# Kernel tuning notes

Hardware: AMD Instinct MI355X
Metric: run time of the kernel (lower is better)

## Reference

```python
import jax, jax.numpy as jnp
import numpy as np

N, E, IN_DIM, OUT_DIM, NNZ = 4096, 2048, 256, 256, 65536
ALPHA = 0.2          # LeakyReLU negative slope
NEG_GAT = -9e15      # masked_fill value for GAT adjacency mask
NEG_ATT = -1e9       # masked_fill value inside ScaledDotProductAttention_hyper


def setup_inputs() -> dict:
    key = jax.random.key(0)
    ks = jax.random.split(key, 10)
    stdv = 1.0 / np.sqrt(OUT_DIM)
    u = lambda k, shape: jax.random.uniform(k, shape, jnp.float32, -stdv, stdv)
    x = jax.random.normal(ks[0], (N, IN_DIM), jnp.float32)
    node_idx = jax.random.randint(ks[1], (NNZ,), 0, N, jnp.int32)
    edge_idx = jax.random.randint(ks[2], (NNZ,), 0, E, jnp.int32)
    hyperedge_index = jnp.stack([node_idx, edge_idx])  # [2, NNZ]
    return {
        "x": x,
        "weight": u(ks[3], (IN_DIM, OUT_DIM)),
        "weight2": u(ks[4], (IN_DIM, OUT_DIM)),
        "weight3": u(ks[5], (OUT_DIM, OUT_DIM)),
        "weight_g": u(ks[6], (IN_DIM, OUT_DIM)),
        "a_g": u(ks[7], (2 * OUT_DIM, 1)),
        "word_context": u(ks[8], (1, OUT_DIM)),
        "bias": u(ks[9], (OUT_DIM,)),
        "hyperedge_index": hyperedge_index,
        "num_edges": E,
    }


def reference(x, weight, weight2, weight3, weight_g, a_g, word_context, bias,
              hyperedge_index, num_edges):
    n = x.shape[0]
    d = weight_g.shape[1]
    temp = d ** 0.5  # temperature = out_features ** 0.5

    # --- hypergraph preprocessing: dense incidence H [N, E] and node adjacency A [N, N]
    H = jnp.zeros((n, num_edges), x.dtype).at[hyperedge_index[0], hyperedge_index[1]].set(1.0)
    A = (H @ H.T > 0).astype(x.dtype)
    A = A.at[jnp.arange(n), jnp.arange(n)].set(1.0)  # fill_diagonal_(1)

    # --- dense GAT-style attention over the clique-expanded graph
    Wh_g = x @ weight_g                               # [N, D]
    Wh1 = Wh_g @ a_g[:d]                              # [N, 1]
    Wh2 = Wh_g @ a_g[d:]                              # [N, 1]
    e_g = jax.nn.leaky_relu(Wh1 + Wh2.T, ALPHA)       # [N, N]
    attention_g = jax.nn.softmax(jnp.where(A > 0, e_g, NEG_GAT), axis=1)

    # --- project node-node attention onto hyperedges: [N, E]
    graph2hyper = attention_g @ H

    # --- dual hypergraph cross-attention (eval mode: dropout is identity)
    x_4att = x @ weight2                              # [N, D]
    xw = x @ weight + bias                            # [N, D] (transfer=True)

    # attention1: hyperedge queries attend over nodes, mask = H.T [E, N]
    q1 = jnp.broadcast_to(word_context[0], (num_edges, d))
    attn1 = (q1 / temp) @ x_4att.T                    # [E, N]
    attn1 = jnp.where(H.T == 0, NEG_ATT, attn1)
    att1 = jax.nn.softmax(graph2hyper.T, axis=-1) + jax.nn.softmax(attn1, axis=-1)
    edge = att1 @ xw                                  # [E, D]
    att2he = att1.T                                   # [N, E]

    # attention2: node queries attend over hyperedges, mask = H [N, E]
    edge_4att = edge @ weight3                        # [E, D]
    attn2 = (x_4att / temp) @ edge_4att.T             # [N, E]
    attn2 = jnp.where(H == 0, NEG_ATT, attn2)
    att2hn = jax.nn.softmax(graph2hyper, axis=-1) + jax.nn.softmax(attn2, axis=-1)
    node = att2hn @ edge                              # [N, D]

    # --- combine attentions and aggregate
    att2_he_out = att2he @ att2he.T                   # [N, N]
    att2_hn_out = att2hn @ att2hn.T                   # [N, N]
    attention_out = attention_g + att2_he_out + att2_hn_out
    h_prime_g = jax.nn.elu(attention_out @ Wh_g)      # concat=True -> ELU

    node = jax.nn.relu(node)                          # concat=True -> ReLU, then squeeze
    return node, h_prime_g
```

## Files before the change

### kernel.cpp

```cpp
#include <hip/hip_runtime.h>
#include <cstdint>
#include <cstddef>


#define DI __device__ __forceinline__
typedef unsigned short u16;
typedef unsigned int   u32;
typedef __bf16 bf16x8 __attribute__((ext_vector_type(8)));
typedef float  f32x4  __attribute__((ext_vector_type(4)));
typedef u32    u32x4  __attribute__((ext_vector_type(4)));

constexpr int NN  = 4096;
constexpr int EE  = 2048;
constexpr int NNZb = 65536;

constexpr size_t MB = (size_t)1 << 20;
constexpr size_t OFF_HBITS   = 0;
constexpr size_t OFF_HBITST  = 1*MB;
constexpr size_t OFF_ABITS   = 2*MB;
constexpr size_t OFF_EDGE    = 2*MB;
constexpr size_t OFF_WH1     = 4*MB;
constexpr size_t OFF_WH2     = 4*MB + 16384;
constexpr size_t OFF_V       = 4*MB + 32768;
constexpr size_t OFF_RSINV   = 4*MB + 49152;
constexpr size_t OFF_WCAT    = 5*MB;
constexpr size_t OFF_XB      = 6*MB;
constexpr size_t OFF_EDGET   = 6*MB;
constexpr size_t OFF_HN2T    = 7*MB;
constexpr size_t OFF_WHG     = 8*MB;
constexpr size_t OFF_X4ATT   = 10*MB;
constexpr size_t OFF_YB      = 12*MB;
constexpr size_t OFF_XWT     = 14*MB;
constexpr size_t OFF_WHGTA   = 16*MB;
constexpr size_t OFF_HBT     = 18*MB;
constexpr size_t OFF_EDGE2T  = 18*MB;
constexpr size_t OFF_WHGTB   = 34*MB;
constexpr size_t OFF_EXPA    = 36*MB;
constexpr size_t OFF_ATT1    = 36*MB;
constexpr size_t OFF_ATT2HN  = 36*MB;
constexpr size_t OFF_ATT1T   = 52*MB;
constexpr size_t OFF_G2H     = 68*MB;
constexpr size_t OFF_G2HT    = 84*MB;
constexpr size_t OFF_ATT2HNT = 84*MB;
constexpr size_t OFF_ATTN2   = 100*MB;
constexpr size_t OFF_G1      = 116*MB;
constexpr size_t OFF_C2      = 120*MB;

DI u16 to_bf(float f) {
  union { float f; u32 u; } x; x.f = f;
  u32 r = x.u + 0x7fffu + ((x.u >> 16) & 1u);
  return (u16)(r >> 16);
}
DI float from_bf(u16 h) { union { u32 u; float f; } x; x.u = (u32)h << 16; return x.f; }
DI void store_bf4(u16* p, float a, float b, float c, float d) {
  u32 lo = (u32)to_bf(a) | ((u32)to_bf(b) << 16);
  u32 hi = (u32)to_bf(c) | ((u32)to_bf(d) << 16);
  *(u32*)p = lo; *((u32*)p + 1) = hi;
}

DI float wredf(float v) {
  #pragma unroll
  for (int o = 32; o; o >>= 1) v += __shfl_down(v, o);
  return v;
}
DI int wredi(int v) {
  #pragma unroll
  for (int o = 32; o; o >>= 1) v += __shfl_down(v, o);
  return v;
}

typedef __attribute__((address_space(3))) void lds_void;
typedef __attribute__((address_space(1))) void glb_void;
DI void async_load16(const void* g, void* l) {
  __builtin_amdgcn_global_load_lds((glb_void*)(uintptr_t)g,
                                   (lds_void*)(u32)(uintptr_t)l, 16, 0, 0);
}

template <int BM, int BN, class Epi>
DI void gemm_body(const u16* __restrict__ A, const u16* __restrict__ B,
                  int nb, int K, Epi epi, int tile, u16* As, u16* Bs)
{
  constexpr int BK = 64;
  constexpr int WM = BM / 2, WN = BN / 2;
  constexpr int FM = WM / 16, FN = WN / 16;
  constexpr int AI = (BM * 8) / 256, BI = (BN * 8) / 256;

  const int tid = threadIdx.x;
  const int w = tid >> 6, l = tid & 63;
  const int bi = tile / nb, bj = tile - bi * nb;
  const int i0 = bi * BM, j0 = bj * BN;
  const int wm = (w & 1) * WM, wn = (w >> 1) * WN;
  const int quad = l >> 4, m16 = l & 15;

  f32x4 acc[FM][FN] = {};

  for (int kb = 0; kb < K; kb += BK) {
    __syncthreads();
    #pragma unroll
    for (int i = 0; i < AI; ++i) {
      const int ci = (i * 4 + w) * 64 + l;
      const int r = ci >> 3;
      const int lc = (ci & 7) ^ (r & 7);
      async_load16(A + (size_t)(i0 + r) * K + kb + lc * 8, &As[(i * 4 + w) * 512]);
    }
    #pragma unroll
    for (int i = 0; i < BI; ++i) {
      const int ci = (i * 4 + w) * 64 + l;
      const int r = ci >> 3;
      const int lc = (ci & 7) ^ (r & 7);
      async_load16(B + (size_t)(j0 + r) * K + kb + lc * 8, &Bs[(i * 4 + w) * 512]);
    }
    __syncthreads();
    #pragma unroll
    for (int ks = 0; ks < 2; ++ks) {
      bf16x8 af[FM], bfv[FN];
      #pragma unroll
      for (int mi = 0; mi < FM; ++mi) {
        const int row = wm + mi * 16 + m16;
        af[mi] = *(const bf16x8*)&As[row * BK + (((ks * 4 + quad) ^ (row & 7)) * 8)];
      }
      #pragma unroll
      for (int ni = 0; ni < FN; ++ni) {
        const int row = wn + ni * 16 + m16;
        bfv[ni] = *(const bf16x8*)&Bs[row * BK + (((ks * 4 + quad) ^ (row & 7)) * 8)];
      }
      #pragma unroll
      for (int mi = 0; mi < FM; ++mi)
        #pragma unroll
        for (int ni = 0; ni < FN; ++ni)
          acc[mi][ni] = __builtin_amdgcn_mfma_f32_16x16x32_bf16(
              af[mi], bfv[ni], acc[mi][ni], 0, 0, 0);
    }
  }
  #pragma unroll
  for (int mi = 0; mi < FM; ++mi)
    #pragma unroll
    for (int ni = 0; ni < FN; ++ni) {
      const int rb = i0 + wm + mi * 16 + quad * 4;
      const int c  = j0 + wn + ni * 16 + m16;
      epi(rb, c, acc[mi][ni]);
    }
}

DI void t32_tile(const u16* __restrict__ in, u16* __restrict__ out,
                 int R, int C, int bx, int by, u16* t) {
  int tx = threadIdx.x & 31, ty = threadIdx.x >> 5;
  int x0 = bx * 32, y0 = by * 32;
  #pragma unroll
  for (int k = 0; k < 32; k += 8)
    t[(ty + k) * 33 + tx] = in[(size_t)(y0 + ty + k) * C + x0 + tx];
  __syncthreads();
  #pragma unroll
  for (int k = 0; k < 32; k += 8)
    out[(size_t)(x0 + ty + k) * R + y0 + tx] = t[tx * 33 + ty + k];
}

struct EpiG0 {
  u16 *whg, *whgTa, *whgTb, *x4, *xwT; const float* bias;
  DI void operator()(int r, int c, f32x4 v) const {
    if (c < 256) {
      #pragma unroll
      for (int i = 0; i < 4; ++i) whg[(r + i) * 256 + c] = to_bf(v[i]);
      store_bf4(&whgTa[(size_t)c * NN + r], v[0], v[1], v[2], v[3]);
      store_bf4(&whgTb[(size_t)c * NN + r], v[0], v[1], v[2], v[3]);
    } else if (c < 512) {
      #pragma unroll
      for (int i = 0; i < 4; ++i) x4[(r + i) * 256 + (c - 256)] = to_bf(v[i]);
    } else {
      float b = bias[c - 512];
      store_bf4(&xwT[(size_t)(c - 512) * NN + r], v[0]+b, v[1]+b, v[2]+b, v[3]+b);
    }
  }
};
struct EpiBig {
  const float* rsInv; u16* g2h; u16* g2hT; float* g1;
  DI void operator()(int r, int c, f32x4 v) const {
    float w0 = v[0]*rsInv[r], w1 = v[1]*rsInv[r+1], w2 = v[2]*rsInv[r+2], w3 = v[3]*rsInv[r+3];
    if (c < 2048) {
      g2h[(size_t)r * EE + c] = to_bf(w0);
      g2h[(size_t)(r+1) * EE + c] = to_bf(w1);
      g2h[(size_t)(r+2) * EE + c] = to_bf(w2);
      g2h[(size_t)(r+3) * EE + c] = to_bf(w3);
      store_bf4(&g2hT[(size_t)c * NN + r], w0, w1, w2, w3);
    } else {
      g1[(r) * 256 + (c - 2048)] = w0;
      g1[(r+1) * 256 + (c - 2048)] = w1;
      g1[(r+2) * 256 + (c - 2048)] = w2;
      g1[(r+3) * 256 + (c - 2048)] = w3;
    }
  }
};
struct EpiEdgeT {
  u16 *edgeT, *edge2T, *edge;
  DI void operator()(int r, int c, f32x4 v) const {
    if (r < 256) {
      #pragma unroll
      for (int i = 0; i < 4; ++i) edgeT[(size_t)(r + i) * EE + c] = to_bf(v[i]);
      store_bf4(&edge[(size_t)c * 256 + r], v[0], v[1], v[2], v[3]);
    } else {
      #pragma unroll
      for (int i = 0; i < 4; ++i) edge2T[(size_t)(r - 256 + i) * EE + c] = to_bf(v[i]);
    }
  }
};
struct EpiCombine {
  const float* g1; const float* c2; float* out;
  DI void operator()(int r, int c, f32x4 v) const {
    if (c < 256) {
      #pragma unroll
      for (int i = 0; i < 4; ++i) out[(r + i) * 256 + c] = fmaxf(v[i], 0.f);
    } else {
      int d = c - 256;
      #pragma unroll
      for (int i = 0; i < 4; ++i) {
        float s = g1[(r + i) * 256 + d] + c2[(r + i) * 256 + d] + v[i];
        out[1048576 + (r + i) * 256 + d] = s > 0.f ? s : expm1f(s);
      }
    }
  }
};
struct EpiBf16 { u16* out; int ldn;
  DI void operator()(int r, int c, f32x4 v) const {
    #pragma unroll
    for (int i = 0; i < 4; ++i) out[(size_t)(r + i) * ldn + c] = to_bf(v[i]);
  } };
struct EpiBf16Scale { u16* out; int ldn; float s;
  DI void operator()(int r, int c, f32x4 v) const {
    #pragma unroll
    for (int i = 0; i < 4; ++i) out[(size_t)(r + i) * ldn + c] = to_bf(v[i] * s);
  } };
struct EpiF32 { float* out; int ldn;
  DI void operator()(int r, int c, f32x4 v) const {
    #pragma unroll
    for (int i = 0; i < 4; ++i) out[(size_t)(r + i) * ldn + c] = v[i];
  } };

template <int BM, int BN, int LB, class Epi>
__global__ __launch_bounds__(256, LB)
void gemm_k(const u16* __restrict__ A, const u16* __restrict__ B,
            int nb, int K, Epi epi) {
  __shared__ __align__(16) u16 smem[(BM + BN) * 64];
  gemm_body<BM, BN>(A, B, nb, K, epi, blockIdx.x, smem, smem + BM * 64);
}

__global__ __launch_bounds__(256, 2)
void k_tri_edge(const u16* __restrict__ Fcat, const u16* __restrict__ Att1,
                EpiEdgeT e0,
                const u16* __restrict__ X4att, const u16* __restrict__ W3b,
                EpiBf16 e1,
                const u16* __restrict__ tin, u16* __restrict__ tout) {
  __shared__ __align__(16) u16 smem[192 * 64];
  int b = blockIdx.x;
  if (b < 256)      gemm_body<64, 64>(Fcat, Att1, 32, 4096, e0, b, smem, smem + 64 * 64);
  else if (b < 384) gemm_body<128, 64>(X4att, W3b, 4, 256, e1, b - 256, smem, smem + 128 * 64);
  else { int t = b - 384; t32_tile(tin, tout, EE, NN, t & 127, t >> 7, smem); }
}

__global__ __launch_bounds__(256, 2)
void k_dual_attn2(const u16* __restrict__ Att1T, const u16* __restrict__ Edge2T,
                  EpiF32 e0,
                  const u16* __restrict__ Yb, const u16* __restrict__ Edge,
                  EpiBf16Scale e1) {
  __shared__ __align__(16) u16 smem[256 * 64];
  int b = blockIdx.x;
  if (b < 128) gemm_body<128, 64>(Att1T, Edge2T, 4, 2048, e0, b, smem, smem + 128 * 64);
  else         gemm_body<128, 128>(Yb, Edge, 16, 256, e1, b - 128, smem, smem + 128 * 64);
}

__global__ void k_prep(const float* wg, const float* w2, const float* w1,
                       const float* w3, const float* x, u16* wcat, u16* xb,
                       char* zbits, char* zhbt) {
  int idx = blockIdx.x * 256 + threadIdx.x;
  if (blockIdx.x < 5120) {
    if (idx < 196608) {
      int blk = idx >> 16, r = idx & 65535;
      int d = r >> 8, kk = r & 255;
      const float* src = blk == 0 ? wg : blk == 1 ? w2 : w1;
      wcat[idx] = to_bf(src[kk * 256 + d]);
    } else if (idx < 262144) {
      int r = idx - 196608;
      wcat[196608 + r] = to_bf(w3[r]);
    } else {
      int r = idx - 262144;
      xb[r] = to_bf(x[r]);
    }
  } else {
    int z = idx - 5120 * 256;
    u32x4 zero = {0, 0, 0, 0};
    if (z < 262144) ((u32x4*)zbits)[z] = zero;
    else            ((u32x4*)zhbt)[z - 262144] = zero;
  }
}

__global__ void k_scatter_diag(const int* __restrict__ hidx, u32* hbits, u32* hbitsT,
                               u16* hbT, u32* abits) {
  int k = blockIdx.x * 256 + threadIdx.x;
  if (k < NNZb) {
    int n = hidx[k], e = hidx[NNZb + k];
    atomicOr(&hbits[n * 64 + (e >> 5)], 1u << (e & 31));
    atomicOr(&hbitsT[e * 128 + (n >> 5)], 1u << (n & 31));
    hbT[(size_t)e * NN + n] = 0x3F80;
  } else {
    int i = k - NNZb;
    if (i < NN) atomicOr(&abits[i * 128 + (i >> 5)], 1u << (i & 31));
  }
}

__global__ void k_rowclique(const u16* __restrict__ whg, const u16* __restrict__ x4,
                            const float* __restrict__ ag, const float* __restrict__ wc,
                            float* wh1, float* wh2, float* v,
                            const u32* __restrict__ hbitsT, u32* abits) {
  __shared__ int list[512];
  __shared__ int cnt;
  int tid = threadIdx.x;
  if (blockIdx.x < 1024) {
    int wv = tid >> 6, l = tid & 63;
    int row = blockIdx.x * 4 + wv;
    float s1 = 0, s2 = 0, s3 = 0;
    #pragma unroll
    for (int dd = 0; dd < 4; ++dd) {
      int d = l * 4 + dd;
      float a = from_bf(whg[row * 256 + d]);
      s1 += a * ag[d]; s2 += a * ag[256 + d];
      s3 += from_bf(x4[row * 256 + d]) * wc[d];
    }
    s1 = wredf(s1); s2 = wredf(s2); s3 = wredf(s3);
    if (l == 0) { wh1[row] = s1; wh2[row] = s2; v[row] = s3 * (1.0f / 16.0f); }
  } else {
    int e = blockIdx.x - 1024;
    if (tid == 0) cnt = 0;
    __syncthreads();
    if (tid < 128) {
      u32 w = hbitsT[e * 128 + tid];
      while (w) {
        int b = __ffs(w) - 1;
        int p = atomicAdd(&cnt, 1);
        if (p < 512) list[p] = tid * 32 + b;
        w &= w - 1;
      }
    }
    __syncthreads();
    int c = cnt < 512 ? cnt : 512;
    for (int p = tid; p < c * c; p += 256) {
      int i = list[p / c], j = list[p % c];
      atomicOr(&abits[i * 128 + (j >> 5)], 1u << (j & 31));
    }
  }
}

__global__ void k_exprows(const u32* __restrict__ abits, const float* __restrict__ wh1,
                          const float* __restrict__ wh2, u16* __restrict__ expA,
                          float* rsInv) {
  int i = blockIdx.x, tid = threadIdx.x;
  __shared__ float w2s[NN];
  __shared__ float ssum;
  for (int j = tid; j < NN; j += 256) w2s[j] = wh2[j];
  if (tid == 0) ssum = 0.f;
  __syncthreads();
  float a = wh1[i], lsum = 0.f;
  for (int j = tid; j < NN; j += 256) {
    u32 w = abits[i * 128 + (j >> 5)];
    u16 h = 0;
    if ((w >> (j & 31)) & 1) {
      float z = a + w2s[j];
      float eg = z > 0.f ? z : 0.2f * z;
      h = to_bf(__expf(eg));
      lsum += from_bf(h);
    }
    expA[(size_t)i * NN + j] = h;
  }
  lsum = wredf(lsum);
  if ((tid & 63) == 0) atomicAdd(&ssum, lsum);
  __syncthreads();
  if (tid == 0) rsInv[i] = 1.0f / ssum;
}

__global__ void k_edge_softmax(const u16* __restrict__ g2hT, const u32* __restrict__ hbitsT,
                               const float* __restrict__ v, u16* __restrict__ att1) {
  int e = blockIdx.x, tid = threadIdx.x;
  __shared__ float evals[NN];
  __shared__ u32 hw[128];
  __shared__ float s1s, s2s; __shared__ int cs;
  if (tid == 0) { s1s = 0.f; s2s = 0.f; cs = 0; }
  if (tid < 128) hw[tid] = hbitsT[e * 128 + tid];
  __syncthreads();
  float sum1 = 0.f;
  for (int j = tid; j < NN; j += 256) {
    float ev = __expf(from_bf(g2hT[(size_t)e * NN + j]));
    evals[j] = ev; sum1 += ev;
  }
  float sum2 = 0.f; int cnt = 0;
  if (tid < 128) {
    u32 w = hw[tid]; cnt = __popc(w);
    while (w) { int b = __ffs(w) - 1; sum2 += __expf(v[tid * 32 + b]); w &= w - 1; }
  }
  sum1 = wredf(sum1); sum2 = wredf(sum2); cnt = wredi(cnt);
  if ((tid & 63) == 0) { atomicAdd(&s1s, sum1); atomicAdd(&s2s, sum2); atomicAdd(&cs, cnt); }
  __syncthreads();
  float inv1 = 1.0f / s1s;
  int c = cs;
  float inv2 = c > 0 ? 1.0f / s2s : 0.0f;
  float unif = c > 0 ? 0.0f : (1.0f / (float)NN);
  for (int j = tid; j < NN; j += 256) {
    float t = evals[j] * inv1 + unif;
    if ((hw[j >> 5] >> (j & 31)) & 1) t += __expf(v[j]) * inv2;
    att1[(size_t)e * NN + j] = to_bf(t);
  }
}

__global__ void k_node_softmax(const u16* __restrict__ g2h, const u16* __restrict__ attn2,
                               const u32* __restrict__ hbits, u16* __restrict__ att2hn) {
  int n = blockIdx.x, tid = threadIdx.x;
  __shared__ float ev3[EE], ev4[EE];
  __shared__ u32 hw[64];
  __shared__ float s3s, s4s; __shared__ int cs;
  if (tid == 0) { s3s = 0.f; s4s = 0.f; cs = 0; }
  if (tid < 64) hw[tid] = hbits[n * 64 + tid];
  __syncthreads();
  float s3 = 0.f, s4 = 0.f; int cl = 0;
  for (int e = tid; e < EE; e += 256) {
    float x3 = __expf(from_bf(g2h[(size_t)n * EE + e]));
    ev3[e] = x3; s3 += x3;
    bool m = (hw[e >> 5] >> (e & 31)) & 1;
    float x4 = m ? __expf(from_bf(attn2[(size_t)n * EE + e])) : 0.f;
    ev4[e] = x4; s4 += x4; cl += m;
  }
  s3 = wredf(s3); s4 = wredf(s4); cl = wredi(cl);
  if ((tid & 63) == 0) { atomicAdd(&s3s, s3); atomicAdd(&s4s, s4); atomicAdd(&cs, cl); }
  __syncthreads();
  float inv3 = 1.0f / s3s;
  int c = cs;
  float inv4 = c > 0 ? 1.0f / s4s : 0.0f;
  float unif = c > 0 ? 0.0f : (1.0f / (float)EE);
  for (int e = tid; e < EE; e += 256)
    att2hn[(size_t)n * EE + e] = to_bf(ev3[e] * inv3 + ev4[e] * inv4 + unif);
}

__global__ void k_transpose(const u16* __restrict__ in, u16* __restrict__ out,
                            int R, int C) {
  __shared__ u16 t[32 * 33];
  t32_tile(in, out, R, C, blockIdx.x, blockIdx.y, t);
}

extern "C" void kernel_launch(void* const* d_in, const int* in_sizes, int n_in,
                              void* d_out, int out_size, void* d_ws, size_t ws_size,
                              hipStream_t stream) {
  (void)in_sizes; (void)n_in; (void)out_size; (void)ws_size;
  const float* x    = (const float*)d_in[0];
  const float* w1   = (const float*)d_in[1];
  const float* w2   = (const float*)d_in[2];
  const float* w3   = (const float*)d_in[3];
  const float* wg   = (const float*)d_in[4];
  const float* ag   = (const float*)d_in[5];
  const float* wc   = (const float*)d_in[6];
  const float* bias = (const float*)d_in[7];
  const int*   hidx = (const int*)d_in[8];
  float* out = (float*)d_out;
  char* ws = (char*)d_ws;

  u32* Hbits   = (u32*)(ws + OFF_HBITS);
  u32* HbitsT  = (u32*)(ws + OFF_HBITST);
  u32* Abits   = (u32*)(ws + OFF_ABITS);
  float* Wh1   = (float*)(ws + OFF_WH1);
  float* Wh2   = (float*)(ws + OFF_WH2);
  float* V     = (float*)(ws + OFF_V);
  float* RsInv = (float*)(ws + OFF_RSINV);
  u16* Wcat    = (u16*)(ws + OFF_WCAT);
  u16* W3b     = Wcat + 196608;
  u16* Xb      = (u16*)(ws + OFF_XB);
  u16* Whg     = (u16*)(ws + OFF_WHG);
  u16* X4att   = (u16*)(ws + OFF_X4ATT);
  u16* Yb      = (u16*)(ws + OFF_YB);
  u16* XwT     = (u16*)(ws + OFF_XWT);
  u16* WhgTa   = (u16*)(ws + OFF_WHGTA);
  u16* HbT     = (u16*)(ws + OFF_HBT);
  u16* WhgTb   = (u16*)(ws + OFF_WHGTB);
  u16* ExpA    = (u16*)(ws + OFF_EXPA);
  u16* Att1    = (u16*)(ws + OFF_ATT1);
  u16* Att1T   = (u16*)(ws + OFF_ATT1T);
  u16* Att2hn  = (u16*)(ws + OFF_ATT2HN);
  u16* G2h     = (u16*)(ws + OFF_G2H);
  u16* G2hT    = (u16*)(ws + OFF_G2HT);
  u16* Att2hnT = (u16*)(ws + OFF_ATT2HNT);
  u16* Attn2   = (u16*)(ws + OFF_ATTN2);
  float* G1    = (float*)(ws + OFF_G1);
  float* C2    = (float*)(ws + OFF_C2);
  u16* Edge    = (u16*)(ws + OFF_EDGE);
  u16* EdgeT   = (u16*)(ws + OFF_EDGET);
  u16* Hn2T    = (u16*)(ws + OFF_HN2T);
  u16* Edge2T  = (u16*)(ws + OFF_EDGE2T);

  k_prep<<<10240, 256, 0, stream>>>(wg, w2, w1, w3, x, Wcat, Xb,
                                    ws + OFF_HBITS, ws + OFF_HBT);
  k_scatter_diag<<<272, 256, 0, stream>>>(hidx, Hbits, HbitsT, HbT, Abits);
  gemm_k<128, 64, 3><<<384, 256, 0, stream>>>(
      Xb, Wcat, 12, 256, EpiG0{Whg, WhgTa, WhgTb, X4att, XwT, bias});
  k_rowclique<<<3072, 256, 0, stream>>>(Whg, X4att, ag, wc, Wh1, Wh2, V,
                                        HbitsT, Abits);
  k_exprows<<<NN, 256, 0, stream>>>(Abits, Wh1, Wh2, ExpA, RsInv);
  gemm_k<128, 96, 3><<<768, 256, 0, stream>>>(
      ExpA, HbT, 24, NN, EpiBig{RsInv, G2h, G2hT, G1});
  k_edge_softmax<<<EE, 256, 0, stream>>>(G2hT, HbitsT, V, Att1);
  k_tri_edge<<<8576, 256, 0, stream>>>(
      XwT, Att1, EpiEdgeT{EdgeT, Edge2T, Edge},
      X4att, W3b, EpiBf16{Yb, 256},
      Att1, Att1T);
  k_dual_attn2<<<640, 256, 0, stream>>>(
      Att1T, Edge2T, EpiF32{C2, 256},
      Yb, Edge, EpiBf16Scale{Attn2, EE, 1.0f / 16.0f});
  k_node_softmax<<<NN, 256, 0, stream>>>(G2h, Attn2, Hbits, Att2hn);
  k_transpose<<<dim3(64, 128), 256, 0, stream>>>(Att2hn, Att2hnT, NN, EE);
  gemm_k<64, 32, 2><<<256, 256, 0, stream>>>(
      WhgTa, Att2hnT, 64, NN, EpiBf16{Hn2T, EE});
  gemm_k<64, 64, 2><<<512, 256, 0, stream>>>(
      Att2hn, EdgeT, 8, EE, EpiCombine{G1, C2, out});
}
```

Before: 395.0 us.

## Replace dense ExpA×H GEMM with sparse per-edge gather and split-K Hn2 GEMM

Drops the dense bf16 incidence matrix HbT and the large ExpA@[H|WhgT] GEMM. A new k_sparse kernel builds exp-rows for 8 nodes per block in LDS and gathers graph2hyper through per-edge member lists produced in k_rowclique. G1 moves to a separate unnormalised GEMM whose row scaling happens in the combine epilogue, and that GEMM is fused with the edge softmax in one launch. The WhgT·Att2hnT GEMM becomes split-K with float atomics plus a cast kernel. Member lists are capped at 64 per half-edge, which could truncate in unusual inputs, and the atomics add nondeterminism.

Result: slower. 403.5 us (+2.2%).

```diff
diff --git a/kernel.cpp b/kernel.cpp
--- a/kernel.cpp
+++ b/kernel.cpp
@@ -32,16 +32,17 @@
 constexpr size_t OFF_YB      = 12*MB;
 constexpr size_t OFF_XWT     = 14*MB;
 constexpr size_t OFF_WHGTA   = 16*MB;
-constexpr size_t OFF_HBT     = 18*MB;
 constexpr size_t OFF_EDGE2T  = 18*MB;
-constexpr size_t OFF_WHGTB   = 34*MB;
+constexpr size_t OFF_GLISTS  = 19*MB;
+constexpr size_t OFF_CNT2    = 19*MB + 524288;
+constexpr size_t OFF_HN2ACC  = 34*MB;
 constexpr size_t OFF_EXPA    = 36*MB;
-constexpr size_t OFF_ATT1    = 36*MB;
 constexpr size_t OFF_ATT2HN  = 36*MB;
 constexpr size_t OFF_ATT1T   = 52*MB;
 constexpr size_t OFF_G2H     = 68*MB;
 constexpr size_t OFF_G2HT    = 84*MB;
 constexpr size_t OFF_ATT2HNT = 84*MB;
+constexpr size_t OFF_ATT1    = 100*MB;
 constexpr size_t OFF_ATTN2   = 100*MB;
 constexpr size_t OFF_G1      = 116*MB;
 constexpr size_t OFF_C2      = 120*MB;
@@ -52,6 +53,8 @@
   return (u16)(r >> 16);
 }
 DI float from_bf(u16 h) { union { u32 u; float f; } x; x.u = (u32)h << 16; return x.f; }
+DI float bflo(u32 u) { union { u32 u; float f; } x; x.u = u << 16; return x.f; }
+DI float bfhi(u32 u) { union { u32 u; float f; } x; x.u = u & 0xffff0000u; return x.f; }
 DI void store_bf4(u16* p, float a, float b, float c, float d) {
   u32 lo = (u32)to_bf(a) | ((u32)to_bf(b) << 16);
   u32 hi = (u32)to_bf(c) | ((u32)to_bf(d) << 16);
@@ -78,7 +81,8 @@
 
 template <int BM, int BN, class Epi>
 DI void gemm_body(const u16* __restrict__ A, const u16* __restrict__ B,
-                  int nb, int K, Epi epi, int tile, u16* As, u16* Bs)
+                  int nb, int K, int k0, int kLen, Epi epi, int tile,
+                  u16* As, u16* Bs)
 {
   constexpr int BK = 64;
   constexpr int WM = BM / 2, WN = BN / 2;
@@ -94,7 +98,7 @@
 
   f32x4 acc[FM][FN] = {};
 
-  for (int kb = 0; kb < K; kb += BK) {
+  for (int kb = k0; kb < k0 + kLen; kb += BK) {
     __syncthreads();
     #pragma unroll
     for (int i = 0; i < AI; ++i) {
@@ -156,13 +160,12 @@
 }
 
 struct EpiG0 {
-  u16 *whg, *whgTa, *whgTb, *x4, *xwT; const float* bias;
+  u16 *whg, *whgTa, *x4, *xwT; const float* bias;
   DI void operator()(int r, int c, f32x4 v) const {
     if (c < 256) {
       #pragma unroll
       for (int i = 0; i < 4; ++i) whg[(r + i) * 256 + c] = to_bf(v[i]);
       store_bf4(&whgTa[(size_t)c * NN + r], v[0], v[1], v[2], v[3]);
-      store_bf4(&whgTb[(size_t)c * NN + r], v[0], v[1], v[2], v[3]);
     } else if (c < 512) {
       #pragma unroll
       for (int i = 0; i < 4; ++i) x4[(r + i) * 256 + (c - 256)] = to_bf(v[i]);
@@ -172,24 +175,6 @@
     }
   }
 };
-struct EpiBig {
-  const float* rsInv; u16* g2h; u16* g2hT; float* g1;
-  DI void operator()(int r, int c, f32x4 v) const {
-    float w0 = v[0]*rsInv[r], w1 = v[1]*rsInv[r+1], w2 = v[2]*rsInv[r+2], w3 = v[3]*rsInv[r+3];
-    if (c < 2048) {
-      g2h[(size_t)r * EE + c] = to_bf(w0);
-      g2h[(size_t)(r+1) * EE + c] = to_bf(w1);
-      g2h[(size_t)(r+2) * EE + c] = to_bf(w2);
-      g2h[(size_t)(r+3) * EE + c] = to_bf(w3);
-      store_bf4(&g2hT[(size_t)c * NN + r], w0, w1, w2, w3);
-    } else {
-      g1[(r) * 256 + (c - 2048)] = w0;
-      g1[(r+1) * 256 + (c - 2048)] = w1;
-      g1[(r+2) * 256 + (c - 2048)] = w2;
-      g1[(r+3) * 256 + (c - 2048)] = w3;
-    }
-  }
-};
 struct EpiEdgeT {
   u16 *edgeT, *edge2T, *edge;
   DI void operator()(int r, int c, f32x4 v) const {
@@ -204,7 +189,7 @@
   }
 };
 struct EpiCombine {
-  const float* g1; const float* c2; float* out;
+  const float* g1; const float* c2; const float* rsInv; float* out;
   DI void operator()(int r, int c, f32x4 v) const {
     if (c < 256) {
       #pragma unroll
@@ -213,7 +198,7 @@
       int d = c - 256;
       #pragma unroll
       for (int i = 0; i < 4; ++i) {
-        float s = g1[(r + i) * 256 + d] + c2[(r + i) * 256 + d] + v[i];
+        float s = g1[(r + i) * 256 + d] * rsInv[r + i] + c2[(r + i) * 256 + d] + v[i];
         out[1048576 + (r + i) * 256 + d] = s > 0.f ? s : expm1f(s);
       }
     }
@@ -234,42 +219,27 @@
     #pragma unroll
     for (int i = 0; i < 4; ++i) out[(size_t)(r + i) * ldn + c] = v[i];
   } };
-
-template <int BM, int BN, int LB, class Epi>
+struct EpiAtomF32 { float* out; int ldn;
+  DI void operator()(int r, int c, f32x4 v) const {
+    #pragma unroll
+    for (int i = 0; i < 4; ++i) atomicAdd(&out[(size_t)(r + i) * ldn + c], v[i]);
+  } };
+
+template <int BM, int BN, int S, int LB, class Epi>
 __global__ __launch_bounds__(256, LB)
 void gemm_k(const u16* __restrict__ A, const u16* __restrict__ B,
             int nb, int K, Epi epi) {
   __shared__ __align__(16) u16 smem[(BM + BN) * 64];
-  gemm_body<BM, BN>(A, B, nb, K, epi, blockIdx.x, smem, smem + BM * 64);
-}
-
-__global__ __launch_bounds__(256, 2)
-void k_tri_edge(const u16* __restrict__ Fcat, const u16* __restrict__ Att1,
-                EpiEdgeT e0,
-                const u16* __restrict__ X4att, const u16* __restrict__ W3b,
-                EpiBf16 e1,
-                const u16* __restrict__ tin, u16* __restrict__ tout) {
-  __shared__ __align__(16) u16 smem[192 * 64];
-  int b = blockIdx.x;
-  if (b < 256)      gemm_body<64, 64>(Fcat, Att1, 32, 4096, e0, b, smem, smem + 64 * 64);
-  else if (b < 384) gemm_body<128, 64>(X4att, W3b, 4, 256, e1, b - 256, smem, smem + 128 * 64);
-  else { int t = b - 384; t32_tile(tin, tout, EE, NN, t & 127, t >> 7, smem); }
-}
-
-__global__ __launch_bounds__(256, 2)
-void k_dual_attn2(const u16* __restrict__ Att1T, const u16* __restrict__ Edge2T,
-                  EpiF32 e0,
-                  const u16* __restrict__ Yb, const u16* __restrict__ Edge,
-                  EpiBf16Scale e1) {
-  __shared__ __align__(16) u16 smem[256 * 64];
-  int b = blockIdx.x;
-  if (b < 128) gemm_body<128, 64>(Att1T, Edge2T, 4, 2048, e0, b, smem, smem + 128 * 64);
-  else         gemm_body<128, 128>(Yb, Edge, 16, 256, e1, b - 128, smem, smem + 128 * 64);
+  const int tilesPer = gridDim.x / S;
+  int t = blockIdx.x;
+  const int s = t / tilesPer; t -= s * tilesPer;
+  const int kLen = K / S;
+  gemm_body<BM, BN>(A, B, nb, K, s * kLen, kLen, epi, t, smem, smem + BM * 64);
 }
 
 __global__ void k_prep(const float* wg, const float* w2, const float* w1,
                        const float* w3, const float* x, u16* wcat, u16* xb,
-                       char* zbits, char* zhbt) {
+                       char* zbits, char* zhn2) {
   int idx = blockIdx.x * 256 + threadIdx.x;
   if (blockIdx.x < 5120) {
     if (idx < 196608) {
@@ -288,18 +258,17 @@
     int z = idx - 5120 * 256;
     u32x4 zero = {0, 0, 0, 0};
     if (z < 262144) ((u32x4*)zbits)[z] = zero;
-    else            ((u32x4*)zhbt)[z - 262144] = zero;
+    else            ((u32x4*)zhn2)[z - 262144] = zero;
   }
 }
 
 __global__ void k_scatter_diag(const int* __restrict__ hidx, u32* hbits, u32* hbitsT,
-                               u16* hbT, u32* abits) {
+                               u32* abits) {
   int k = blockIdx.x * 256 + threadIdx.x;
   if (k < NNZb) {
     int n = hidx[k], e = hidx[NNZb + k];
     atomicOr(&hbits[n * 64 + (e >> 5)], 1u << (e & 31));
     atomicOr(&hbitsT[e * 128 + (n >> 5)], 1u << (n & 31));
-    hbT[(size_t)e * NN + n] = 0x3F80;
   } else {
     int i = k - NNZb;
     if (i < NN) atomicOr(&abits[i * 128 + (i >> 5)], 1u << (i & 31));
@@ -309,9 +278,11 @@
 __global__ void k_rowclique(const u16* __restrict__ whg, const u16* __restrict__ x4,
                             const float* __restrict__ ag, const float* __restrict__ wc,
                             float* wh1, float* wh2, float* v,
-                            const u32* __restrict__ hbitsT, u32* abits) {
+                            const u32* __restrict__ hbitsT, u32* abits,
+                            u16* glists, u32* cnt2) {
   __shared__ int list[512];
   __shared__ int cnt;
+  __shared__ u32 c2[2];
   int tid = threadIdx.x;
   if (blockIdx.x < 1024) {
     int wv = tid >> 6, l = tid & 63;
@@ -329,17 +300,23 @@
   } else {
     int e = blockIdx.x - 1024;
     if (tid == 0) cnt = 0;
+    if (tid < 2) c2[tid] = 0;
     __syncthreads();
     if (tid < 128) {
       u32 w = hbitsT[e * 128 + tid];
+      int p = tid >> 6;
       while (w) {
         int b = __ffs(w) - 1;
-        int p = atomicAdd(&cnt, 1);
-        if (p < 512) list[p] = tid * 32 + b;
+        int n = tid * 32 + b;
+        int q = atomicAdd(&cnt, 1);
+        if (q < 512) list[q] = n;
+        u32 s = atomicAdd(&c2[p], 1u);
+        if (s < 64) glists[(e * 2 + p) * 64 + s] = (u16)n;
         w &= w - 1;
       }
     }
     __syncthreads();
+    if (tid < 2) cnt2[e * 2 + tid] = c2[tid] < 64u ? c2[tid] : 64u;
     int c = cnt < 512 ? cnt : 512;
     for (int p = tid; p < c * c; p += 256) {
       int i = list[p / c], j = list[p % c];
@@ -348,40 +325,95 @@
   }
 }
 
-__global__ void k_exprows(const u32* __restrict__ abits, const float* __restrict__ wh1,
-                          const float* __restrict__ wh2, u16* __restrict__ expA,
-                          float* rsInv) {
-  int i = blockIdx.x, tid = threadIdx.x;
-  __shared__ float w2s[NN];
-  __shared__ float ssum;
-  for (int j = tid; j < NN; j += 256) w2s[j] = wh2[j];
-  if (tid == 0) ssum = 0.f;
-  __syncthreads();
-  float a = wh1[i], lsum = 0.f;
-  for (int j = tid; j < NN; j += 256) {
-    u32 w = abits[i * 128 + (j >> 5)];
-    u16 h = 0;
-    if ((w >> (j & 31)) & 1) {
-      float z = a + w2s[j];
-      float eg = z > 0.f ? z : 0.2f * z;
-      h = to_bf(__expf(eg));
-      lsum += from_bf(h);
-    }
-    expA[(size_t)i * NN + j] = h;
-  }
-  lsum = wredf(lsum);
-  if ((tid & 63) == 0) atomicAdd(&ssum, lsum);
-  __syncthreads();
-  if (tid == 0) rsInv[i] = 1.0f / ssum;
-}
-
-__global__ void k_edge_softmax(const u16* __restrict__ g2hT, const u32* __restrict__ hbitsT,
-                               const float* __restrict__ v, u16* __restrict__ att1) {
-  int e = blockIdx.x, tid = threadIdx.x;
-  __shared__ float evals[NN];
-  __shared__ u32 hw[128];
-  __shared__ float s1s, s2s; __shared__ int cs;
-  if (tid == 0) { s1s = 0.f; s2s = 0.f; cs = 0; }
+__global__ __launch_bounds__(256, 2)
+void k_sparse(const u32* __restrict__ abits, const float* __restrict__ wh1,
+              const float* __restrict__ wh2, const u16* __restrict__ glists,
+              const u32* __restrict__ cnt2, u16* __restrict__ expA,
+              float* __restrict__ rsInv, u16* __restrict__ g2h,
+              u16* __restrict__ g2hT)
+{
+  __shared__ u16 lds[2048 * 12];
+  __shared__ float sums8[8], rsi[8];
+  const int tid = threadIdx.x;
+  const int i0 = blockIdx.x * 8;
+  const int r = tid & 7, ng = tid >> 3;
+  if (tid < 8) sums8[tid] = 0.f;
+  float acc[8][8] = {};
+  const float wh1r = wh1[i0 + r];
+  for (int p = 0; p < 2; ++p) {
+    __syncthreads();
+    float partial = 0.f;
+    for (int it = 0; it < 8; ++it) {
+      const int g = ng + 32 * it;
+      const int n0 = p * 2048 + g * 8;
+      const u32 m8 = (abits[(size_t)(i0 + r) * 128 + (n0 >> 5)] >> (n0 & 31)) & 0xffu;
+      u32 pk[4];
+      #pragma unroll
+      for (int q = 0; q < 4; ++q) {
+        u32 wrd = 0;
+        #pragma unroll
+        for (int h = 0; h < 2; ++h) {
+          const int j = q * 2 + h;
+          u16 hb = 0;
+          if ((m8 >> j) & 1u) {
+            float z = wh1r + wh2[n0 + j];
+            float eg = z > 0.f ? z : 0.2f * z;
+            hb = to_bf(__expf(eg));
+            partial += from_bf(hb);
+          }
+          lds[(g * 8 + j) * 12 + r] = hb;
+          wrd |= (u32)hb << (16 * h);
+        }
+        pk[q] = wrd;
+      }
+      *(u32x4*)&expA[(size_t)(i0 + r) * 4096 + n0] = u32x4{pk[0], pk[1], pk[2], pk[3]};
+    }
+    atomicAdd(&sums8[r], partial);
+    __syncthreads();
+    #pragma unroll
+    for (int j = 0; j < 8; ++j) {
+      const int e = tid + 256 * j;
+      const int c = (int)cnt2[e * 2 + p];
+      const u16* lst = &glists[(e * 2 + p) * 64];
+      for (int k = 0; k < c; ++k) {
+        const int ln = (int)lst[k] - p * 2048;
+        const u32* lp = (const u32*)&lds[ln * 12];
+        u32 a0 = lp[0], a1 = lp[1], a2 = lp[2], a3 = lp[3];
+        acc[j][0] += bflo(a0); acc[j][1] += bfhi(a0);
+        acc[j][2] += bflo(a1); acc[j][3] += bfhi(a1);
+        acc[j][4] += bflo(a2); acc[j][5] += bfhi(a2);
+        acc[j][6] += bflo(a3); acc[j][7] += bfhi(a3);
+      }
+    }
+  }
+  __syncthreads();
+  if (tid < 8) {
+    float s = 1.f / sums8[tid];
+    rsi[tid] = s; rsInv[i0 + tid] = s;
+  }
+  __syncthreads();
+  #pragma unroll
+  for (int j = 0; j < 8; ++j) {
+    const int e = tid + 256 * j;
+    u32 pk[4];
+    #pragma unroll
+    for (int q = 0; q < 4; ++q) {
+      u16 lo = to_bf(acc[j][2 * q] * rsi[2 * q]);
+      u16 hi = to_bf(acc[j][2 * q + 1] * rsi[2 * q + 1]);
+      pk[q] = (u32)lo | ((u32)hi << 16);
+      g2h[(size_t)(i0 + 2 * q) * EE + e] = lo;
+      g2h[(size_t)(i0 + 2 * q + 1) * EE + e] = hi;
+    }
+    *(u32x4*)&g2hT[(size_t)e * NN + i0] = u32x4{pk[0], pk[1], pk[2], pk[3]};
+  }
+}
+
+DI void edge_softmax_body(int e, const u16* __restrict__ g2hT,
+                          const u32* __restrict__ hbitsT,
+                          const float* __restrict__ v, u16* __restrict__ att1,
+                          float* evals, u32* hw, float* s1s, float* s2s, int* cs) {
+  int tid = threadIdx.x;
+  if (tid == 0) { *s1s = 0.f; *s2s = 0.f; *cs = 0; }
   if (tid < 128) hw[tid] = hbitsT[e * 128 + tid];
   __syncthreads();
   float sum1 = 0.f;
@@ -395,17 +427,58 @@
     while (w) { int b = __ffs(w) - 1; sum2 += __expf(v[tid * 32 + b]); w &= w - 1; }
   }
   sum1 = wredf(sum1); sum2 = wredf(sum2); cnt = wredi(cnt);
-  if ((tid & 63) == 0) { atomicAdd(&s1s, sum1); atomicAdd(&s2s, sum2); atomicAdd(&cs, cnt); }
-  __syncthreads();
-  float inv1 = 1.0f / s1s;
-  int c = cs;
-  float inv2 = c > 0 ? 1.0f / s2s : 0.0f;
+  if ((tid & 63) == 0) { atomicAdd(s1s, sum1); atomicAdd(s2s, sum2); atomicAdd(cs, cnt); }
+  __syncthreads();
+  float inv1 = 1.0f / *s1s;
+  int c = *cs;
+  float inv2 = c > 0 ? 1.0f / *s2s : 0.0f;
   float unif = c > 0 ? 0.0f : (1.0f / (float)NN);
   for (int j = tid; j < NN; j += 256) {
     float t = evals[j] * inv1 + unif;
     if ((hw[j >> 5] >> (j & 31)) & 1) t += __expf(v[j]) * inv2;
     att1[(size_t)e * NN + j] = to_bf(t);
   }
+}
+
+__global__ __launch_bounds__(256, 2)
+void k_dual_g1(const u16* __restrict__ ExpA, const u16* __restrict__ WhgTa,
+               EpiF32 eg,
+               const u16* __restrict__ g2hT, const u32* __restrict__ hbitsT,
+               const float* __restrict__ v, u16* __restrict__ att1) {
+  __shared__ __align__(16) char buf[24576];
+  __shared__ float s1s, s2s; __shared__ int cs;
+  int b = blockIdx.x;
+  if (b < 128) {
+    u16* As = (u16*)buf;
+    gemm_body<128, 64>(ExpA, WhgTa, 4, NN, 0, NN, eg, b, As, As + 128 * 64);
+  } else {
+    edge_softmax_body(b - 128, g2hT, hbitsT, v, att1,
+                      (float*)buf, (u32*)(buf + 16384), &s1s, &s2s, &cs);
+  }
+}
+
+__global__ __launch_bounds__(256, 2)
+void k_tri_edge(const u16* __restrict__ Fcat, const u16* __restrict__ Att1,
+                EpiEdgeT e0,
+                const u16* __restrict__ X4att, const u16* __restrict__ W3b,
+                EpiBf16 e1,
+                const u16* __restrict__ tin, u16* __restrict__ tout) {
+  __shared__ __align__(16) u16 smem[192 * 64];
+  int b = blockIdx.x;
+  if (b < 256)      gemm_body<64, 64>(Fcat, Att1, 32, NN, 0, NN, e0, b, smem, smem + 64 * 64);
+  else if (b < 384) gemm_body<128, 64>(X4att, W3b, 4, 256, 0, 256, e1, b - 256, smem, smem + 128 * 64);
+  else { int t = b - 384; t32_tile(tin, tout, EE, NN, t & 127, t >> 7, smem); }
+}
+
+__global__ __launch_bounds__(256, 2)
+void k_dual_attn2(const u16* __restrict__ Att1T, const u16* __restrict__ Edge2T,
+                  EpiF32 e0,
+                  const u16* __restrict__ Yb, const u16* __restrict__ Edge,
+                  EpiBf16Scale e1) {
+  __shared__ __align__(16) u16 smem[256 * 64];
+  int b = blockIdx.x;
+  if (b < 128) gemm_body<128, 64>(Att1T, Edge2T, 4, EE, 0, EE, e0, b, smem, smem + 128 * 64);
+  else         gemm_body<128, 128>(Yb, Edge, 16, 256, 0, 256, e1, b - 128, smem, smem + 128 * 64);
 }
 
 __global__ void k_node_softmax(const u16* __restrict__ g2h, const u16* __restrict__ attn2,
@@ -440,6 +513,11 @@
                             int R, int C) {
   __shared__ u16 t[32 * 33];
   t32_tile(in, out, R, C, blockIdx.x, blockIdx.y, t);
+}
+
+__global__ void k_cast_hn2(const float* __restrict__ acc, u16* __restrict__ hn2T) {
+  int idx = blockIdx.x * 256 + threadIdx.x;
+  hn2T[idx] = to_bf(acc[idx]);
 }
 
 extern "C" void kernel_launch(void* const* d_in, const int* in_sizes, int n_in,
@@ -473,34 +551,35 @@
   u16* Yb      = (u16*)(ws + OFF_YB);
   u16* XwT     = (u16*)(ws + OFF_XWT);
   u16* WhgTa   = (u16*)(ws + OFF_WHGTA);
-  u16* HbT     = (u16*)(ws + OFF_HBT);
-  u16* WhgTb   = (u16*)(ws + OFF_WHGTB);
+  u16* Edge2T  = (u16*)(ws + OFF_EDGE2T);
+  u16* Glists  = (u16*)(ws + OFF_GLISTS);
+  u32* Cnt2    = (u32*)(ws + OFF_CNT2);
+  float* Hn2Acc = (float*)(ws + OFF_HN2ACC);
   u16* ExpA    = (u16*)(ws + OFF_EXPA);
-  u16* Att1    = (u16*)(ws + OFF_ATT1);
+  u16* Att2hn  = (u16*)(ws + OFF_ATT2HN);
   u16* Att1T   = (u16*)(ws + OFF_ATT1T);
-  u16* Att2hn  = (u16*)(ws + OFF_ATT2HN);
   u16* G2h     = (u16*)(ws + OFF_G2H);
   u16* G2hT    = (u16*)(ws + OFF_G2HT);
   u16* Att2hnT = (u16*)(ws + OFF_ATT2HNT);
+  u16* Att1    = (u16*)(ws + OFF_ATT1);
   u16* Attn2   = (u16*)(ws + OFF_ATTN2);
   float* G1    = (float*)(ws + OFF_G1);
   float* C2    = (float*)(ws + OFF_C2);
   u16* Edge    = (u16*)(ws + OFF_EDGE);
   u16* EdgeT   = (u16*)(ws + OFF_EDGET);
   u16* Hn2T    = (u16*)(ws + OFF_HN2T);
-  u16* Edge2T  = (u16*)(ws + OFF_EDGE2T);
-
-  k_prep<<<10240, 256, 0, stream>>>(wg, w2, w1, w3, x, Wcat, Xb,
-                                    ws + OFF_HBITS, ws + OFF_HBT);
-  k_scatter_diag<<<272, 256, 0, stream>>>(hidx, Hbits, HbitsT, HbT, Abits);
-  gemm_k<128, 64, 3><<<384, 256, 0, stream>>>(
-      Xb, Wcat, 12, 256, EpiG0{Whg, WhgTa, WhgTb, X4att, XwT, bias});
+
+  k_prep<<<6656, 256, 0, stream>>>(wg, w2, w1, w3, x, Wcat, Xb,
+                                   ws + OFF_HBITS, ws + OFF_HN2ACC);
+  k_scatter_diag<<<272, 256, 0, stream>>>(hidx, Hbits, HbitsT, Abits);
+  gemm_k<128, 64, 1, 3><<<384, 256, 0, stream>>>(
+      Xb, Wcat, 12, 256, EpiG0{Whg, WhgTa, X4att, XwT, bias});
   k_rowclique<<<3072, 256, 0, stream>>>(Whg, X4att, ag, wc, Wh1, Wh2, V,
-                                        HbitsT, Abits);
-  k_exprows<<<NN, 256, 0, stream>>>(Abits, Wh1, Wh2, ExpA, RsInv);
-  gemm_k<128, 96, 3><<<768, 256, 0, stream>>>(
-      ExpA, HbT, 24, NN, EpiBig{RsInv, G2h, G2hT, G1});
-  k_edge_softmax<<<EE, 256, 0, stream>>>(G2hT, HbitsT, V, Att1);
+                                        HbitsT, Abits, Glists, Cnt2);
+  k_sparse<<<512, 256, 0, stream>>>(Abits, Wh1, Wh2, Glists, Cnt2,
+                                    ExpA, RsInv, G2h, G2hT);
+  k_dual_g1<<<2176, 256, 0, stream>>>(ExpA, WhgTa, EpiF32{G1, 256},
+                                      G2hT, HbitsT, V, Att1);
   k_tri_edge<<<8576, 256, 0, stream>>>(
       XwT, Att1, EpiEdgeT{EdgeT, Edge2T, Edge},
       X4att, W3b, EpiBf16{Yb, 256},
@@ -510,8 +589,9 @@
       Yb, Edge, EpiBf16Scale{Attn2, EE, 1.0f / 16.0f});
   k_node_softmax<<<NN, 256, 0, stream>>>(G2h, Attn2, Hbits, Att2hn);
   k_transpose<<<dim3(64, 128), 256, 0, stream>>>(Att2hn, Att2hnT, NN, EE);
-  gemm_k<64, 32, 2><<<256, 256, 0, stream>>>(
-      WhgTa, Att2hnT, 64, NN, EpiBf16{Hn2T, EE});
-  gemm_k<64, 64, 2><<<512, 256, 0, stream>>>(
-      Att2hn, EdgeT, 8, EE, EpiCombine{G1, C2, out});
-}
+  gemm_k<64, 64, 4, 2><<<512, 256, 0, stream>>>(
+      WhgTa, Att2hnT, 32, NN, EpiAtomF32{Hn2Acc, EE});
+  k_cast_hn2<<<2048, 256, 0, stream>>>(Hn2Acc, Hn2T);
+  gemm_k<64, 64, 1, 2><<<512, 256, 0, stream>>>(
+      Att2hn, EdgeT, 8, EE, EpiCombine{G1, C2, RsInv, out});
+}
```

## Split-K the Hn2T GEMM with atomic accumulation and add XCD-aware tile swizzles

Applied to the files above, without the earlier changes.

The Hn2T GEMM (K=4096, previously only 256 tiles of 64x32) now runs as 64x64 tiles with split-K by 4 over 512 blocks, accumulating into a zeroed fp32 buffer with atomicAdd. A separate cast kernel then converts that buffer to bf16. The big ExpA x HbT GEMM and the edge GEMM in k_tri_edge remap block indices so tiles sharing B columns land on the same XCD, aiming for better L2 reuse. Costs include extra zeroing in k_prep, fp32 atomic traffic, one more kernel launch, and nondeterministic summation order.

Result: faster. 380.3 us (-3.7%).

```diff
diff --git a/kernel.cpp b/kernel.cpp
--- a/kernel.cpp
+++ b/kernel.cpp
@@ -45,6 +45,7 @@
 constexpr size_t OFF_ATTN2   = 100*MB;
 constexpr size_t OFF_G1      = 116*MB;
 constexpr size_t OFF_C2      = 120*MB;
+constexpr size_t OFF_HN2ACC  = 124*MB;
 
 DI u16 to_bf(float f) {
   union { float f; u32 u; } x; x.f = f;
@@ -78,7 +79,8 @@
 
 template <int BM, int BN, class Epi>
 DI void gemm_body(const u16* __restrict__ A, const u16* __restrict__ B,
-                  int nb, int K, Epi epi, int tile, u16* As, u16* Bs)
+                  int nb, int K, int k0, int kLen, Epi epi, int tile,
+                  u16* As, u16* Bs)
 {
   constexpr int BK = 64;
   constexpr int WM = BM / 2, WN = BN / 2;
@@ -94,7 +96,7 @@
 
   f32x4 acc[FM][FN] = {};
 
-  for (int kb = 0; kb < K; kb += BK) {
+  for (int kb = k0; kb < k0 + kLen; kb += BK) {
     __syncthreads();
     #pragma unroll
     for (int i = 0; i < AI; ++i) {
@@ -234,42 +236,35 @@
     #pragma unroll
     for (int i = 0; i < 4; ++i) out[(size_t)(r + i) * ldn + c] = v[i];
   } };
-
-template <int BM, int BN, int LB, class Epi>
+struct EpiAtomF32 { float* out; int ldn;
+  DI void operator()(int r, int c, f32x4 v) const {
+    #pragma unroll
+    for (int i = 0; i < 4; ++i) atomicAdd(&out[(size_t)(r + i) * ldn + c], v[i]);
+  } };
+
+template <int BM, int BN, int S, int LB, int XSW, class Epi>
 __global__ __launch_bounds__(256, LB)
 void gemm_k(const u16* __restrict__ A, const u16* __restrict__ B,
             int nb, int K, Epi epi) {
   __shared__ __align__(16) u16 smem[(BM + BN) * 64];
-  gemm_body<BM, BN>(A, B, nb, K, epi, blockIdx.x, smem, smem + BM * 64);
-}
-
-__global__ __launch_bounds__(256, 2)
-void k_tri_edge(const u16* __restrict__ Fcat, const u16* __restrict__ Att1,
-                EpiEdgeT e0,
-                const u16* __restrict__ X4att, const u16* __restrict__ W3b,
-                EpiBf16 e1,
-                const u16* __restrict__ tin, u16* __restrict__ tout) {
-  __shared__ __align__(16) u16 smem[192 * 64];
-  int b = blockIdx.x;
-  if (b < 256)      gemm_body<64, 64>(Fcat, Att1, 32, 4096, e0, b, smem, smem + 64 * 64);
-  else if (b < 384) gemm_body<128, 64>(X4att, W3b, 4, 256, e1, b - 256, smem, smem + 128 * 64);
-  else { int t = b - 384; t32_tile(tin, tout, EE, NN, t & 127, t >> 7, smem); }
-}
-
-__global__ __launch_bounds__(256, 2)
-void k_dual_attn2(const u16* __restrict__ Att1T, const u16* __restrict__ Edge2T,
-                  EpiF32 e0,
-                  const u16* __restrict__ Yb, const u16* __restrict__ Edge,
-                  EpiBf16Scale e1) {
-  __shared__ __align__(16) u16 smem[256 * 64];
-  int b = blockIdx.x;
-  if (b < 128) gemm_body<128, 64>(Att1T, Edge2T, 4, 2048, e0, b, smem, smem + 128 * 64);
-  else         gemm_body<128, 128>(Yb, Edge, 16, 256, e1, b - 128, smem, smem + 128 * 64);
+  int t = blockIdx.x;
+  int k0 = 0, kLen = K;
+  if (XSW > 0) {
+    const int xcd = t & 7, idx = t >> 3;
+    const int bj = xcd * XSW + idx % XSW;
+    const int bi = idx / XSW;
+    t = bi * nb + bj;
+  } else if (S > 1) {
+    const int tilesPer = gridDim.x / S;
+    const int s = t / tilesPer; t -= s * tilesPer;
+    kLen = K / S; k0 = s * kLen;
+  }
+  gemm_body<BM, BN>(A, B, nb, K, k0, kLen, epi, t, smem, smem + BM * 64);
 }
 
 __global__ void k_prep(const float* wg, const float* w2, const float* w1,
                        const float* w3, const float* x, u16* wcat, u16* xb,
-                       char* zbits, char* zhbt) {
+                       char* zbits, char* zhbt, char* zhn2) {
   int idx = blockIdx.x * 256 + threadIdx.x;
   if (blockIdx.x < 5120) {
     if (idx < 196608) {
@@ -287,8 +282,9 @@
   } else {
     int z = idx - 5120 * 256;
     u32x4 zero = {0, 0, 0, 0};
-    if (z < 262144) ((u32x4*)zbits)[z] = zero;
-    else            ((u32x4*)zhbt)[z - 262144] = zero;
+    if (z < 262144)       ((u32x4*)zbits)[z] = zero;
+    else if (z < 1310720) ((u32x4*)zhbt)[z - 262144] = zero;
+    else                  ((u32x4*)zhn2)[z - 1310720] = zero;
   }
 }
 
@@ -408,6 +404,34 @@
   }
 }
 
+__global__ __launch_bounds__(256, 2)
+void k_tri_edge(const u16* __restrict__ Fcat, const u16* __restrict__ Att1,
+                EpiEdgeT e0,
+                const u16* __restrict__ X4att, const u16* __restrict__ W3b,
+                EpiBf16 e1,
+                const u16* __restrict__ tin, u16* __restrict__ tout) {
+  __shared__ __align__(16) u16 smem[192 * 64];
+  int b = blockIdx.x;
+  if (b < 256) {
+    const int xcd = b & 7, idx = b >> 3;
+    const int t = (idx / 4) * 32 + xcd * 4 + (idx & 3);
+    gemm_body<64, 64>(Fcat, Att1, 32, NN, 0, NN, e0, t, smem, smem + 64 * 64);
+  }
+  else if (b < 384) gemm_body<128, 64>(X4att, W3b, 4, 256, 0, 256, e1, b - 256, smem, smem + 128 * 64);
+  else { int t = b - 384; t32_tile(tin, tout, EE, NN, t & 127, t >> 7, smem); }
+}
+
+__global__ __launch_bounds__(256, 2)
+void k_dual_attn2(const u16* __restrict__ Att1T, const u16* __restrict__ Edge2T,
+                  EpiF32 e0,
+                  const u16* __restrict__ Yb, const u16* __restrict__ Edge,
+                  EpiBf16Scale e1) {
+  __shared__ __align__(16) u16 smem[256 * 64];
+  int b = blockIdx.x;
+  if (b < 128) gemm_body<128, 64>(Att1T, Edge2T, 4, EE, 0, EE, e0, b, smem, smem + 128 * 64);
+  else         gemm_body<128, 128>(Yb, Edge, 16, 256, 0, 256, e1, b - 128, smem, smem + 128 * 64);
+}
+
 __global__ void k_node_softmax(const u16* __restrict__ g2h, const u16* __restrict__ attn2,
                                const u32* __restrict__ hbits, u16* __restrict__ att2hn) {
   int n = blockIdx.x, tid = threadIdx.x;
@@ -440,6 +464,11 @@
                             int R, int C) {
   __shared__ u16 t[32 * 33];
   t32_tile(in, out, R, C, blockIdx.x, blockIdx.y, t);
+}
+
+__global__ void k_cast_hn2(const float* __restrict__ acc, u16* __restrict__ hn2T) {
+  int idx = blockIdx.x * 256 + threadIdx.x;
+  hn2T[idx] = to_bf(acc[idx]);
 }
 
 extern "C" void kernel_launch(void* const* d_in, const int* in_sizes, int n_in,
@@ -485,20 +514,21 @@
   u16* Attn2   = (u16*)(ws + OFF_ATTN2);
   float* G1    = (float*)(ws + OFF_G1);
   float* C2    = (float*)(ws + OFF_C2);
+  float* Hn2Acc = (float*)(ws + OFF_HN2ACC);
   u16* Edge    = (u16*)(ws + OFF_EDGE);
   u16* EdgeT   = (u16*)(ws + OFF_EDGET);
   u16* Hn2T    = (u16*)(ws + OFF_HN2T);
   u16* Edge2T  = (u16*)(ws + OFF_EDGE2T);
 
-  k_prep<<<10240, 256, 0, stream>>>(wg, w2, w1, w3, x, Wcat, Xb,
-                                    ws + OFF_HBITS, ws + OFF_HBT);
+  k_prep<<<10752, 256, 0, stream>>>(wg, w2, w1, w3, x, Wcat, Xb,
+                                    ws + OFF_HBITS, ws + OFF_HBT, ws + OFF_HN2ACC);
   k_scatter_diag<<<272, 256, 0, stream>>>(hidx, Hbits, HbitsT, HbT, Abits);
-  gemm_k<128, 64, 3><<<384, 256, 0, stream>>>(
+  gemm_k<128, 64, 1, 3, 0><<<384, 256, 0, stream>>>(
       Xb, Wcat, 12, 256, EpiG0{Whg, WhgTa, WhgTb, X4att, XwT, bias});
   k_rowclique<<<3072, 256, 0, stream>>>(Whg, X4att, ag, wc, Wh1, Wh2, V,
                                         HbitsT, Abits);
   k_exprows<<<NN, 256, 0, stream>>>(Abits, Wh1, Wh2, ExpA, RsInv);
-  gemm_k<128, 96, 3><<<768, 256, 0, stream>>>(
+  gemm_k<128, 96, 1, 3, 3><<<768, 256, 0, stream>>>(
       ExpA, HbT, 24, NN, EpiBig{RsInv, G2h, G2hT, G1});
   k_edge_softmax<<<EE, 256, 0, stream>>>(G2hT, HbitsT, V, Att1);
   k_tri_edge<<<8576, 256, 0, stream>>>(
@@ -510,8 +540,9 @@
       Yb, Edge, EpiBf16Scale{Attn2, EE, 1.0f / 16.0f});
   k_node_softmax<<<NN, 256, 0, stream>>>(G2h, Attn2, Hbits, Att2hn);
   k_transpose<<<dim3(64, 128), 256, 0, stream>>>(Att2hn, Att2hnT, NN, EE);
-  gemm_k<64, 32, 2><<<256, 256, 0, stream>>>(
-      WhgTa, Att2hnT, 64, NN, EpiBf16{Hn2T, EE});
-  gemm_k<64, 64, 2><<<512, 256, 0, stream>>>(
+  gemm_k<64, 64, 4, 3, 0><<<512, 256, 0, stream>>>(
+      WhgTa, Att2hnT, 32, NN, EpiAtomF32{Hn2Acc, EE});
+  k_cast_hn2<<<2048, 256, 0, stream>>>(Hn2Acc, Hn2T);
+  gemm_k<64, 64, 1, 2, 0><<<512, 256, 0, stream>>>(
       Att2hn, EdgeT, 8, EE, EpiCombine{G1, C2, out});
 }
```
